# Kernel tuning notes

Hardware: AMD Instinct MI355X
Metric: run time of the kernel (lower is better)

Reference implementation:

```python
import jax, jax.numpy as jnp
import numpy as np
import math

H, D, DEG = 8, 64, 2
GATE_BIAS = 6.906768

def _rope(x, sin, cos):
    # GPT-J style interleaved rotary: even lanes = x1*cos - x2*sin, odd = x2*cos + x1*sin
    x1, x2 = x[..., ::2], x[..., 1::2]
    s = sin[None, :, None, :]
    c = cos[None, :, None, :]
    even = x1 * c - x2 * s
    odd = x2 * c + x1 * s
    return jnp.stack([even, odd], axis=-1).reshape(x.shape)

def _forward(x, w_attn, w_proj):
    B, T, C = x.shape
    h, d, deg = H, D, DEG
    hd = h * d
    scale = 1.0 / math.sqrt(d)
    qkvg = x @ w_attn                                   # (B,T,3hd+h)
    q = qkvg[..., :hd].reshape(B, T, h, d)
    k = qkvg[..., hd:2 * hd].reshape(B, T, h, d)
    v = qkvg[..., 2 * hd:3 * hd].reshape(B, T, h, d)
    log_g = jax.nn.log_sigmoid(GATE_BIAS + qkvg[..., 3 * hd:].astype(jnp.float32))  # (B,T,h)
    # sinusoidal RoPE with frequency 2*pi / T**(2i/d), as in get_sinusoidal_embeddings
    pos = jnp.arange(T, dtype=jnp.float32)
    div = 2.0 * math.pi / (float(T) ** (jnp.arange(0, d, 2, dtype=jnp.float32) / d))
    ang = pos[:, None] * div[None, :]                   # (T, d//2)
    sin, cos = jnp.sin(ang), jnp.cos(ang)
    q = _rope(q, sin, cos)
    k = _rope(k, sin, cos)
    # gated symmetric-power attention: quadratic reference of chunked power_full
    # score_ts = (scale * q_t . k_s)^deg * exp(L_t - L_s), causal, row-normalized
    L = jnp.cumsum(log_g, axis=1).transpose(0, 2, 1)    # (B,h,T) cumulative log-gates
    qk = jnp.einsum('bthd,bshd->bhts', q, k) * scale    # (B,h,T,T)
    log_gate = L[:, :, :, None] - L[:, :, None, :]      # L_t - L_s
    causal = jnp.tril(jnp.ones((T, T), dtype=bool))
    scores = jnp.where(causal, (qk ** deg) * jnp.exp(log_gate), 0.0)
    denom = jnp.maximum(scores.sum(-1, keepdims=True), 1e-6)
    y = jnp.einsum('bhts,bshd->bthd', scores / denom, v)  # (B,T,h,d)
    return y.reshape(B, T, hd) @ w_proj

def setup_inputs() -> dict:
    key = jax.random.key(0)
    k1, k2, k3 = jax.random.split(key, 3)
    B, T, C = 2, 2048, 512
    x = jax.random.normal(k1, (B, T, C), dtype=jnp.float32)
    w_attn = jax.random.normal(k2, (C, 3 * H * D + H), dtype=jnp.float32) * 0.02
    w_proj = jax.random.normal(k3, (H * D, C), dtype=jnp.float32) * 0.02
    return {"x": x, "w_attn": w_attn, "w_proj": w_proj}

def reference(x, w_attn, w_proj):
    return _forward(x, w_attn, w_proj)
```

## Files before the change

kernel.cpp:

```cpp
#include <hip/hip_runtime.h>
#include <math.h>

constexpr int B_ = 2, T_ = 2048, C_ = 512, H_ = 8, D_ = 64;
constexpr int QKVG_ = 3 * H_ * D_ + H_;
constexpr float GATE_BIAS_ = 6.906768f;
constexpr int NPAD1_ = 1664;
constexpr int SC_ = 8;
constexpr int NBLK_ = 1280;
constexpr int MC_ = 4096 * 512;
constexpr int BHT_ = B_ * H_ * T_;

typedef __attribute__((ext_vector_type(8))) short short8;
typedef __attribute__((ext_vector_type(4))) float f32x4;

__device__ __forceinline__ unsigned short f2b(float f) {
    unsigned int u = __float_as_uint(f);
    unsigned int r = (u + 0x7fffu + ((u >> 16) & 1u)) >> 16;
    return (unsigned short)r;
}
__device__ __forceinline__ short8 pack8(float4 a, float4 b) {
    short8 r;
    r[0] = (short)f2b(a.x); r[1] = (short)f2b(a.y);
    r[2] = (short)f2b(a.z); r[3] = (short)f2b(a.w);
    r[4] = (short)f2b(b.x); r[5] = (short)f2b(b.y);
    r[6] = (short)f2b(b.z); r[7] = (short)f2b(b.w);
    return r;
}

__device__ __forceinline__ void gl2lds16(const unsigned short* g, void* lds_base) {
    __builtin_amdgcn_global_load_lds(
        (const __attribute__((address_space(1))) unsigned int*)g,
        (__attribute__((address_space(3))) unsigned int*)lds_base, 16, 0, 0);
}

__device__ __forceinline__ void packT_body(
    const float* __restrict__ W, unsigned short* __restrict__ Bt,
    int K, int N, int nt, int kt, int tid, float (*Ws)[65])
{
    {
        const int r = tid >> 2;
        const int c0 = (tid & 3) * 16;
#pragma unroll
        for (int j = 0; j < 16; ++j) {
            const int n = nt + c0 + j;
            Ws[r][c0 + j] = (n < N) ? W[(size_t)(kt + r) * N + n] : 0.f;
        }
    }
    __syncthreads();
    {
        const int d = tid >> 2;
        const int cc = tid & 3;
        const int kc = cc * 16;
        short8 o0, o1;
#pragma unroll
        for (int j = 0; j < 8; ++j) o0[j] = (short)f2b(Ws[kc + j][d]);
#pragma unroll
        for (int j = 0; j < 8; ++j) o1[j] = (short)f2b(Ws[kc + 8 + j][d]);
        const int row = nt + d;
        unsigned short* op = Bt + (size_t)row * K + kt;
        *(short8*)(op + ((2 * cc) ^ (row & 7)) * 8)     = o0;
        *(short8*)(op + ((2 * cc + 1) ^ (row & 7)) * 8) = o1;
    }
}

__global__ __launch_bounds__(256) void pack_inputs(
    const float* __restrict__ x, const float* __restrict__ w_attn,
    const float* __restrict__ w_proj, unsigned short* __restrict__ xb,
    unsigned short* __restrict__ Bt1, unsigned short* __restrict__ Bt2)
{
    __shared__ float Ws[64][65];
    const int bid = blockIdx.x;
    const int tid = threadIdx.x;
    if (bid < 1024) {
        const int i = bid * 256 + tid;
        float4 f0 = *(const float4*)(x + (size_t)i * 8);
        float4 f1 = *(const float4*)(x + (size_t)i * 8 + 4);
        const int row = i >> 6;
        const int ic = i & 63;
        const int swc = (ic & ~7) | ((ic & 7) ^ (row & 7));
        *(short8*)(xb + (size_t)row * 512 + swc * 8) = pack8(f0, f1);
    } else if (bid < 1232) {
        const int q = bid - 1024;
        packT_body(w_attn, Bt1, C_, QKVG_, (q % 26) * 64, (q / 26) * 64, tid, Ws);
    } else {
        const int q = bid - 1232;
        packT_body(w_proj, Bt2, H_ * D_, C_, (q & 7) * 64, (q >> 3) * 64, tid, Ws);
    }
}

__global__ __launch_bounds__(256) void gemm_bf16(
    const unsigned short* __restrict__ A, const unsigned short* __restrict__ Bt,
    float* __restrict__ C, int M, int N, int K)
{
    __shared__ __align__(16) char AsB[128 * 128];
    __shared__ __align__(16) char BsB[128 * 128];

    const int tid = threadIdx.x;
    const int wave = tid >> 6, lane = tid & 63;
    const int l15 = lane & 15, lhi = lane >> 4;
    const int wr = wave >> 1, wc = wave & 1;
    const int bm = blockIdx.y * 128, bn = blockIdx.x * 128;

    f32x4 acc[4][4];
#pragma unroll
    for (int i = 0; i < 4; ++i)
#pragma unroll
        for (int j = 0; j < 4; ++j) acc[i][j] = (f32x4){0.f, 0.f, 0.f, 0.f};

    const unsigned short* Arow = A + (size_t)bm * K;
    const unsigned short* Brow = Bt + (size_t)bn * K;
    const int sw = (l15 & 7) << 4;

    const int srow = tid >> 3;
    const int schunk = tid & 7;

    for (int k0 = 0; k0 < K; k0 += 64) {
        __syncthreads();
#pragma unroll
        for (int p = 0; p < 4; ++p) {
            const int row = p * 32 + srow;
            const size_t goff = (size_t)row * K + k0 + schunk * 8;
            gl2lds16(Arow + goff, AsB + p * 4096 + wave * 1024);
            gl2lds16(Brow + goff, BsB + p * 4096 + wave * 1024);
        }
        __syncthreads();

        short8 af[4][2];
#pragma unroll
        for (int mi = 0; mi < 4; ++mi) {
            const int row = wr * 64 + mi * 16 + l15;
#pragma unroll
            for (int kk = 0; kk < 2; ++kk)
                af[mi][kk] = *(const short8*)(AsB + row * 128 + ((kk * 64 + lhi * 16) ^ sw));
        }
#pragma unroll
        for (int ni = 0; ni < 4; ++ni) {
            const int row = wc * 64 + ni * 16 + l15;
            short8 bf0 = *(const short8*)(BsB + row * 128 + ((lhi * 16) ^ sw));
            short8 bf1 = *(const short8*)(BsB + row * 128 + ((64 + lhi * 16) ^ sw));
#pragma unroll
            for (int mi = 0; mi < 4; ++mi) {
                acc[mi][ni] = __builtin_amdgcn_mfma_f32_16x16x32_bf16(af[mi][0], bf0, acc[mi][ni], 0, 0, 0);
                acc[mi][ni] = __builtin_amdgcn_mfma_f32_16x16x32_bf16(af[mi][1], bf1, acc[mi][ni], 0, 0, 0);
            }
        }
    }

#pragma unroll
    for (int mi = 0; mi < 4; ++mi) {
        const int gm = bm + wr * 64 + mi * 16 + lhi * 4;
#pragma unroll
        for (int r = 0; r < 4; ++r) {
            float* crow = C + (size_t)(gm + r) * N;
#pragma unroll
            for (int ni = 0; ni < 4; ++ni) {
                const int gn = bn + wc * 64 + ni * 16 + l15;
                if (gn < N) crow[gn] = acc[mi][ni][r];
            }
        }
    }
}

__global__ __launch_bounds__(256) void gate_cumsum(
    const float* __restrict__ qkvg, float* __restrict__ Lg)
{
    __shared__ float wsum[4];
    const int bh = blockIdx.x;
    const int b = bh >> 3, h = bh & 7;
    const int tid = threadIdx.x;
    const int lane = tid & 63, wv = tid >> 6;

    const float* gp = qkvg + (size_t)(b * T_ + tid * 8) * QKVG_ + 1536 + h;
    float v[8];
    float s = 0.f;
#pragma unroll
    for (int j = 0; j < 8; ++j) {
        const float z = gp[(size_t)j * QKVG_] + GATE_BIAS_;
        const float lg = (z > 0.f) ? -log1pf(expf(-z)) : (z - log1pf(expf(z)));
        s += lg;
        v[j] = s;
    }
    float ssum = s;
#pragma unroll
    for (int off = 1; off < 64; off <<= 1) {
        float n = __shfl_up(ssum, off, 64);
        if (lane >= off) ssum += n;
    }
    if (lane == 63) wsum[wv] = ssum;
    __syncthreads();
    float base = ssum - s;
#pragma unroll
    for (int w = 0; w < 3; ++w)
        base += (w < wv) ? wsum[w] : 0.f;

    float* op = Lg + (size_t)bh * T_ + tid * 8;
#pragma unroll
    for (int j = 0; j < 8; ++j) op[j] = v[j] + base;
}

__global__ __launch_bounds__(256) void qkv_pack(
    const float* __restrict__ qkvg, const float* __restrict__ Lg,
    unsigned short* __restrict__ Qsb, unsigned short* __restrict__ Ksb,
    unsigned short* __restrict__ Vtb)
{
    __shared__ float Vs[64][68];
    const int tid = threadIdx.x;
    const int stile = blockIdx.x;
    const int bh = blockIdx.y;
    const int b = bh >> 3, h = bh & 7;
    const int r = tid >> 2, c = tid & 3;
    const int t = stile * 64 + r;

    float sn[8], cs[8];
#pragma unroll
    for (int j = 0; j < 8; ++j) {
        const int i = c * 8 + j;
        const float div = 6.2831853071795864f * exp2f((float)i * (-11.0f / 32.0f));
        const float ang = (float)t * div;
        sn[j] = sinf(ang);
        cs[j] = cosf(ang);
    }

    const float Lt = Lg[(size_t)bh * T_ + t];
    const float eQ = __expf(0.5f * Lt) * 0.125f;
    const float eK = __expf(-0.5f * Lt);
    const float* basep = qkvg + (size_t)(b * T_ + t) * QKVG_ + h * 64 + c * 16;

    {
        float q[16];
        *(float4*)&q[0]  = *(const float4*)(basep + 0);
        *(float4*)&q[4]  = *(const float4*)(basep + 4);
        *(float4*)&q[8]  = *(const float4*)(basep + 8);
        *(float4*)&q[12] = *(const float4*)(basep + 12);
#pragma unroll
        for (int j = 0; j < 8; ++j) {
            const float x1 = q[2 * j], x2 = q[2 * j + 1];
            q[2 * j]     = (x1 * cs[j] - x2 * sn[j]) * eQ;
            q[2 * j + 1] = (x2 * cs[j] + x1 * sn[j]) * eQ;
        }
        unsigned short* op = Qsb + ((size_t)bh * T_ + t) * 64 + c * 16;
        *(short8*)(op + 0) = pack8(*(float4*)&q[0], *(float4*)&q[4]);
        *(short8*)(op + 8) = pack8(*(float4*)&q[8], *(float4*)&q[12]);
    }
    {
        float k[16];
        *(float4*)&k[0]  = *(const float4*)(basep + 512);
        *(float4*)&k[4]  = *(const float4*)(basep + 516);
        *(float4*)&k[8]  = *(const float4*)(basep + 520);
        *(float4*)&k[12] = *(const float4*)(basep + 524);
#pragma unroll
        for (int j = 0; j < 8; ++j) {
            const float x1 = k[2 * j], x2 = k[2 * j + 1];
            k[2 * j]     = (x1 * cs[j] - x2 * sn[j]) * eK;
            k[2 * j + 1] = (x2 * cs[j] + x1 * sn[j]) * eK;
        }
        unsigned short* op = Ksb + ((size_t)bh * T_ + t) * 64;
        *(short8*)(op + ((2 * c) ^ (t & 7)) * 8)     = pack8(*(float4*)&k[0], *(float4*)&k[4]);
        *(short8*)(op + ((2 * c + 1) ^ (t & 7)) * 8) = pack8(*(float4*)&k[8], *(float4*)&k[12]);
    }
    {
        *(float4*)&Vs[r][c * 16 + 0]  = *(const float4*)(basep + 1024);
        *(float4*)&Vs[r][c * 16 + 4]  = *(const float4*)(basep + 1028);
        *(float4*)&Vs[r][c * 16 + 8]  = *(const float4*)(basep + 1032);
        *(float4*)&Vs[r][c * 16 + 12] = *(const float4*)(basep + 1036);
    }
    __syncthreads();
    {
        const int d = tid >> 2, cc = tid & 3;
        short8 o0, o1;
#pragma unroll
        for (int j = 0; j < 8; ++j) o0[j] = (short)f2b(Vs[cc * 16 + j][d]);
#pragma unroll
        for (int j = 0; j < 8; ++j) o1[j] = (short)f2b(Vs[cc * 16 + 8 + j][d]);
        unsigned short* op = Vtb + ((size_t)bh * 64 + d) * T_ + stile * 64;
        *(short8*)(op + ((2 * cc) ^ (d & 7)) * 8)     = o0;
        *(short8*)(op + ((2 * cc + 1) ^ (d & 7)) * 8) = o1;
    }
}

__global__ __launch_bounds__(256) void attn_mfma(
    const unsigned short* __restrict__ Qsb, const unsigned short* __restrict__ Ksb,
    const unsigned short* __restrict__ Vtb,
    float* __restrict__ Y0, float* __restrict__ Yp, float* __restrict__ Dpart)
{
    __shared__ __align__(16) char smem[24576];
    char* KsB = smem;
    char* VtB = smem + 8192;
    char* PsB = smem + 16384;

    const int wg = blockIdx.x;
    const int xcd = wg & 7;
    const int slot = wg >> 3;
    const int bh = (slot < 80) ? xcd : 8 + xcd;
    const int rem = (slot < 80) ? slot : slot - 80;
    const int rr = 79 - rem;
    int bt, sc;
    if (rr < 8)       { bt = rr; sc = 0; }
    else if (rr < 24) { const int q = rr - 8;  bt = 8 + (q >> 1);  sc = q & 1; }
    else if (rr < 48) { const int q = rr - 24; bt = 16 + q / 3;    sc = q % 3; }
    else              { const int q = rr - 48; bt = 24 + (q >> 2); sc = q & 3; }
    const int st0 = sc * SC_;
    const int st1 = min(st0 + SC_ - 1, bt);

    const int tid = threadIdx.x;
    const int wave = tid >> 6;
    const int lane = tid & 63;
    const int l15 = lane & 15;
    const int lhi = lane >> 4;
    const int b = bh >> 3, h = bh & 7;
    const int t0 = bt * 64;

    const int qrow = t0 + wave * 16 + l15;
    const unsigned short* qpp = Qsb + ((size_t)bh * T_ + qrow) * 64 + lhi * 8;
    short8 qf[2];
    qf[0] = *(const short8*)(qpp);
    qf[1] = *(const short8*)(qpp + 32);

    f32x4 accY[4];
#pragma unroll
    for (int n = 0; n < 4; ++n) accY[n] = (f32x4){0.f, 0.f, 0.f, 0.f};
    float den[4] = {0.f, 0.f, 0.f, 0.f};

    const int kchunk = lhi * 16;
    const int rsw = (l15 & 7) << 4;
    const int srow = tid >> 3;
    const int schunk = tid & 7;

    for (int st = st0; st <= st1; ++st) {
        __syncthreads();
#pragma unroll
        for (int p = 0; p < 2; ++p) {
            const int row = p * 32 + srow;
            gl2lds16(Ksb + ((size_t)bh * T_ + st * 64 + row) * 64 + schunk * 8,
                     KsB + p * 4096 + wave * 1024);
            gl2lds16(Vtb + ((size_t)bh * 64 + row) * T_ + st * 64 + schunk * 8,
                     VtB + p * 4096 + wave * 1024);
        }
        __syncthreads();

        f32x4 accS[4];
#pragma unroll
        for (int n = 0; n < 4; ++n) accS[n] = (f32x4){0.f, 0.f, 0.f, 0.f};
#pragma unroll
        for (int n = 0; n < 4; ++n) {
#pragma unroll
            for (int kk = 0; kk < 2; ++kk) {
                short8 bf = *(const short8*)(KsB + (n * 16 + l15) * 128 + ((kk * 64 + kchunk) ^ rsw));
                accS[n] = __builtin_amdgcn_mfma_f32_16x16x32_bf16(qf[kk], bf, accS[n], 0, 0, 0);
            }
        }

        const bool last = (st == bt);
        char* PsW = PsB + wave * 2048;
#pragma unroll
        for (int n = 0; n < 4; ++n) {
#pragma unroll
            for (int r = 0; r < 4; ++r) {
                const float a = accS[n][r];
                float p = a * a;
                if (last)
                    p = ((n * 16 + l15) <= wave * 16 + lhi * 4 + r) ? p : 0.f;
                den[r] += p;
                const int prow = lhi * 4 + r;
                *(unsigned short*)(PsW + prow * 128 + ((2 * (n * 16 + l15)) ^ ((prow & 7) << 4))) = f2b(p);
            }
        }

        short8 pa[2];
#pragma unroll
        for (int kk = 0; kk < 2; ++kk)
            pa[kk] = *(const short8*)(PsW + l15 * 128 + ((kk * 64 + kchunk) ^ rsw));
#pragma unroll
        for (int n = 0; n < 4; ++n) {
#pragma unroll
            for (int kk = 0; kk < 2; ++kk) {
                short8 vb = *(const short8*)(VtB + (n * 16 + l15) * 128 + ((kk * 64 + kchunk) ^ rsw));
                accY[n] = __builtin_amdgcn_mfma_f32_16x16x32_bf16(pa[kk], vb, accY[n], 0, 0, 0);
            }
        }
    }

#pragma unroll
    for (int r = 0; r < 4; ++r) {
        den[r] += __shfl_xor(den[r], 1, 64);
        den[r] += __shfl_xor(den[r], 2, 64);
        den[r] += __shfl_xor(den[r], 4, 64);
        den[r] += __shfl_xor(den[r], 8, 64);
    }

    float* Ybase = (sc == 0) ? Y0 : (Yp + (size_t)(sc - 1) * MC_);
    float* Dbase = Dpart + (size_t)sc * BHT_;
#pragma unroll
    for (int r = 0; r < 4; ++r) {
        const int t = t0 + wave * 16 + lhi * 4 + r;
        if (l15 == 0)
            Dbase[(size_t)bh * T_ + t] = den[r];
        float* yo = Ybase + (size_t)(b * T_ + t) * (H_ * D_) + h * 64 + l15;
#pragma unroll
        for (int n = 0; n < 4; ++n)
            yo[n * 16] = accY[n][r];
    }
}

__global__ __launch_bounds__(256) void normalize_kernel(
    const float* __restrict__ Y0, const float* __restrict__ Yp,
    const float* __restrict__ Dpart, unsigned short* __restrict__ ybb)
{
    const int gid = blockIdx.x * 256 + threadIdx.x;
    const size_t base = (size_t)gid * 8;
    const int row = (int)(base >> 9);
    const int col = (int)(base & 511);
    const int b = row >> 11, t = row & 2047, h = col >> 6;
    const int bh = b * H_ + h;
    const int nsc = ((t >> 6) >> 3) + 1;

    float d = Dpart[(size_t)bh * T_ + t];
    float4 f0 = *(const float4*)(Y0 + base);
    float4 f1 = *(const float4*)(Y0 + base + 4);
    for (int s = 1; s < nsc; ++s) {
        d += Dpart[(size_t)s * BHT_ + (size_t)bh * T_ + t];
        const float* yp = Yp + (size_t)(s - 1) * MC_ + base;
        float4 g0 = *(const float4*)(yp);
        float4 g1 = *(const float4*)(yp + 4);
        f0.x += g0.x; f0.y += g0.y; f0.z += g0.z; f0.w += g0.w;
        f1.x += g1.x; f1.y += g1.y; f1.z += g1.z; f1.w += g1.w;
    }
    const float inv = 1.0f / fmaxf(d, 1e-6f);
    f0.x *= inv; f0.y *= inv; f0.z *= inv; f0.w *= inv;
    f1.x *= inv; f1.y *= inv; f1.z *= inv; f1.w *= inv;

    const int ic = col >> 3;
    const int swc = (ic & ~7) | ((ic & 7) ^ (row & 7));
    *(short8*)(ybb + (size_t)row * 512 + swc * 8) = pack8(f0, f1);
}

extern "C" void kernel_launch(void* const* d_in, const int* in_sizes, int n_in,
                              void* d_out, int out_size, void* d_ws, size_t ws_size,
                              hipStream_t stream)
{
    const float* x      = (const float*)d_in[0];
    const float* w_attn = (const float*)d_in[1];
    const float* w_proj = (const float*)d_in[2];
    float* out = (float*)d_out;

    float* qkvg = (float*)d_ws;
    float* Lg    = qkvg + (size_t)B_ * T_ * QKVG_;
    float* Dpart = Lg + BHT_;
    unsigned short* Vtb = (unsigned short*)(Dpart + 4 * BHT_);
    unsigned short* Bt1 = Vtb + (size_t)B_ * H_ * D_ * T_;
    unsigned short* Bt2 = Bt1 + (size_t)NPAD1_ * C_;
    unsigned short* xb  = Bt2 + (size_t)C_ * C_;
    unsigned short* Ksb = xb;
    unsigned short* ybb = xb;
    float* Yp = (float*)(xb + (size_t)MC_);
    unsigned short* Qsb = (unsigned short*)(Yp + 3 * (size_t)MC_);

    const int M = B_ * T_;

    pack_inputs<<<1296, 256, 0, stream>>>(x, w_attn, w_proj, xb, Bt1, Bt2);

    gemm_bf16<<<dim3(NPAD1_ / 128, M / 128), 256, 0, stream>>>(
        xb, Bt1, qkvg, M, QKVG_, C_);

    gate_cumsum<<<B_ * H_, 256, 0, stream>>>(qkvg, Lg);

    qkv_pack<<<dim3(T_ / 64, B_ * H_), 256, 0, stream>>>(qkvg, Lg, Qsb, Ksb, Vtb);

    attn_mfma<<<NBLK_, 256, 0, stream>>>(Qsb, Ksb, Vtb, out, Yp, Dpart);

    normalize_kernel<<<(MC_ / 8) / 256, 256, 0, stream>>>(out, Yp, Dpart, ybb);

    gemm_bf16<<<dim3(C_ / 128, M / 128), 256, 0, stream>>>(
        ybb, Bt2, out, M, C_, H_ * D_);
}
```

Before: 89.60 us.

## Fuse RoPE, gate scaling and QKV packing into the QKV GEMM epilogue

The gate projection is computed separately in fp32 inside the pack kernel, and a sin/cos table is precomputed there. The gate cumsum now runs before the QKV GEMM, which applies RoPE, the exp(±L/2) scaling and the bf16 packing of Q/K/V directly in its epilogue. This drops the fp32 qkvg intermediate and the separate qkv_pack launch, and the N padding shrinks from 1664 to 1536. In exchange the GEMM epilogue gets heavier, with two LDS staging rounds, and the gate GEMV re-reads x in fp32.

Result: faster. 84.24 us (-6.0%).

```diff
diff --git a/kernel.cpp b/kernel.cpp
--- a/kernel.cpp
+++ b/kernel.cpp
@@ -4,7 +4,7 @@
 constexpr int B_ = 2, T_ = 2048, C_ = 512, H_ = 8, D_ = 64;
 constexpr int QKVG_ = 3 * H_ * D_ + H_;
 constexpr float GATE_BIAS_ = 6.906768f;
-constexpr int NPAD1_ = 1664;
+constexpr int N1_ = 1536;
 constexpr int SC_ = 8;
 constexpr int NBLK_ = 1280;
 constexpr int MC_ = 4096 * 512;
@@ -35,7 +35,7 @@
 
 __device__ __forceinline__ void packT_body(
     const float* __restrict__ W, unsigned short* __restrict__ Bt,
-    int K, int N, int nt, int kt, int tid, float (*Ws)[65])
+    int K, int N, int ldW, int nt, int kt, int tid, float (*Ws)[65])
 {
     {
         const int r = tid >> 2;
@@ -43,7 +43,7 @@
 #pragma unroll
         for (int j = 0; j < 16; ++j) {
             const int n = nt + c0 + j;
-            Ws[r][c0 + j] = (n < N) ? W[(size_t)(kt + r) * N + n] : 0.f;
+            Ws[r][c0 + j] = (n < N) ? W[(size_t)(kt + r) * ldW + n] : 0.f;
         }
     }
     __syncthreads();
@@ -66,9 +66,11 @@
 __global__ __launch_bounds__(256) void pack_inputs(
     const float* __restrict__ x, const float* __restrict__ w_attn,
     const float* __restrict__ w_proj, unsigned short* __restrict__ xb,
-    unsigned short* __restrict__ Bt1, unsigned short* __restrict__ Bt2)
-{
-    __shared__ float Ws[64][65];
+    unsigned short* __restrict__ Bt1, unsigned short* __restrict__ Bt2,
+    float2* __restrict__ sincos, float* __restrict__ g)
+{
+    __shared__ float SM[64 * 65];
+    float (*Ws)[65] = (float(*)[65])SM;
     const int bid = blockIdx.x;
     const int tid = threadIdx.x;
     if (bid < 1024) {
@@ -79,21 +81,98 @@
         const int ic = i & 63;
         const int swc = (ic & ~7) | ((ic & 7) ^ (row & 7));
         *(short8*)(xb + (size_t)row * 512 + swc * 8) = pack8(f0, f1);
-    } else if (bid < 1232) {
+    } else if (bid < 1216) {
         const int q = bid - 1024;
-        packT_body(w_attn, Bt1, C_, QKVG_, (q % 26) * 64, (q / 26) * 64, tid, Ws);
+        packT_body(w_attn, Bt1, C_, N1_, QKVG_, (q % 24) * 64, (q / 24) * 64, tid, Ws);
+    } else if (bid < 1280) {
+        const int q = bid - 1216;
+        packT_body(w_proj, Bt2, H_ * D_, C_, C_, (q & 7) * 64, (q >> 3) * 64, tid, Ws);
+    } else if (bid < 1288) {
+        const int t = (bid - 1280) * 256 + tid;
+        float2* op = sincos + (size_t)t * 32;
+#pragma unroll
+        for (int i = 0; i < 32; ++i) {
+            const float div = 6.2831853071795864f * exp2f((float)i * (-11.0f / 32.0f));
+            const float ang = (float)t * div;
+            op[i] = make_float2(cosf(ang), sinf(ang));
+        }
     } else {
-        const int q = bid - 1232;
-        packT_body(w_proj, Bt2, H_ * D_, C_, (q & 7) * 64, (q >> 3) * 64, tid, Ws);
-    }
-}
-
-__global__ __launch_bounds__(256) void gemm_bf16(
+        const int q = bid - 1288;
+        float* LDSw = SM;
+        {
+            const int k = tid * 2;
+#pragma unroll
+            for (int kk = 0; kk < 2; ++kk) {
+                const float* wp = w_attn + (size_t)(k + kk) * QKVG_ + 1536;
+                float4 wa = *(const float4*)wp;
+                float4 wb = *(const float4*)(wp + 4);
+                float* dst = LDSw + (k + kk) * 8;
+                *(float4*)dst = wa;
+                *(float4*)(dst + 4) = wb;
+            }
+        }
+        __syncthreads();
+        const int m = q * 32 + (tid >> 3);
+        const int h = tid & 7;
+        const float* xrow = x + (size_t)m * C_;
+        float s = 0.f;
+#pragma unroll 4
+        for (int k0 = 0; k0 < 512; k0 += 4) {
+            float4 xv = *(const float4*)(xrow + k0);
+            s += xv.x * LDSw[(k0 + 0) * 8 + h] + xv.y * LDSw[(k0 + 1) * 8 + h]
+               + xv.z * LDSw[(k0 + 2) * 8 + h] + xv.w * LDSw[(k0 + 3) * 8 + h];
+        }
+        const int b = m >> 11, t = m & 2047;
+        g[(size_t)(b * 8 + h) * T_ + t] = s;
+    }
+}
+
+__global__ __launch_bounds__(256) void gate_cumsum(
+    const float* __restrict__ g, float* __restrict__ Lg)
+{
+    __shared__ float wsum[4];
+    const int bh = blockIdx.x;
+    const int tid = threadIdx.x;
+    const int lane = tid & 63, wv = tid >> 6;
+
+    const float* gp = g + (size_t)bh * T_ + tid * 8;
+    float v[8];
+    float s = 0.f;
+#pragma unroll
+    for (int j = 0; j < 8; ++j) {
+        const float z = gp[j] + GATE_BIAS_;
+        const float lg = (z > 0.f) ? -log1pf(expf(-z)) : (z - log1pf(expf(z)));
+        s += lg;
+        v[j] = s;
+    }
+    float ssum = s;
+#pragma unroll
+    for (int off = 1; off < 64; off <<= 1) {
+        float n = __shfl_up(ssum, off, 64);
+        if (lane >= off) ssum += n;
+    }
+    if (lane == 63) wsum[wv] = ssum;
+    __syncthreads();
+    float base = ssum - s;
+#pragma unroll
+    for (int w = 0; w < 3; ++w)
+        base += (w < wv) ? wsum[w] : 0.f;
+
+    float* op = Lg + (size_t)bh * T_ + tid * 8;
+#pragma unroll
+    for (int j = 0; j < 8; ++j) op[j] = v[j] + base;
+}
+
+__global__ __launch_bounds__(256) void gemm_fused(
     const unsigned short* __restrict__ A, const unsigned short* __restrict__ Bt,
-    float* __restrict__ C, int M, int N, int K)
-{
-    __shared__ __align__(16) char AsB[128 * 128];
-    __shared__ __align__(16) char BsB[128 * 128];
+    const float* __restrict__ Lg, const float2* __restrict__ sincos,
+    unsigned short* __restrict__ Qsb, unsigned short* __restrict__ Ksb,
+    unsigned short* __restrict__ Vtb)
+{
+    __shared__ __align__(16) char smem[33280];
+    char* AsB = smem;
+    char* BsB = smem + 16384;
+    float (*epi)[65] = (float(*)[65])smem;
 
     const int tid = threadIdx.x;
     const int wave = tid >> 6, lane = tid & 63;
@@ -107,10 +186,130 @@
 #pragma unroll
         for (int j = 0; j < 4; ++j) acc[i][j] = (f32x4){0.f, 0.f, 0.f, 0.f};
 
+    const unsigned short* Arow = A + (size_t)bm * C_;
+    const unsigned short* Brow = Bt + (size_t)bn * C_;
+    const int sw = (l15 & 7) << 4;
+    const int srow = tid >> 3;
+    const int schunk = tid & 7;
+
+    for (int k0 = 0; k0 < C_; k0 += 64) {
+        __syncthreads();
+#pragma unroll
+        for (int p = 0; p < 4; ++p) {
+            const int row = p * 32 + srow;
+            const size_t goff = (size_t)row * C_ + k0 + schunk * 8;
+            gl2lds16(Arow + goff, AsB + p * 4096 + wave * 1024);
+            gl2lds16(Brow + goff, BsB + p * 4096 + wave * 1024);
+        }
+        __syncthreads();
+
+        short8 af[4][2];
+#pragma unroll
+        for (int mi = 0; mi < 4; ++mi) {
+            const int row = wr * 64 + mi * 16 + l15;
+#pragma unroll
+            for (int kk = 0; kk < 2; ++kk)
+                af[mi][kk] = *(const short8*)(AsB + row * 128 + ((kk * 64 + lhi * 16) ^ sw));
+        }
+#pragma unroll
+        for (int ni = 0; ni < 4; ++ni) {
+            const int row = wc * 64 + ni * 16 + l15;
+            short8 bf0 = *(const short8*)(BsB + row * 128 + ((lhi * 16) ^ sw));
+            short8 bf1 = *(const short8*)(BsB + row * 128 + ((64 + lhi * 16) ^ sw));
+#pragma unroll
+            for (int mi = 0; mi < 4; ++mi) {
+                acc[mi][ni] = __builtin_amdgcn_mfma_f32_16x16x32_bf16(af[mi][0], bf0, acc[mi][ni], 0, 0, 0);
+                acc[mi][ni] = __builtin_amdgcn_mfma_f32_16x16x32_bf16(af[mi][1], bf1, acc[mi][ni], 0, 0, 0);
+            }
+        }
+    }
+
+    const int rid = bn >> 9;
+    const int b = bm >> 11;
+    const int tloc0 = bm & 2047;
+
+#pragma unroll
+    for (int hc = 0; hc < 2; ++hc) {
+        __syncthreads();
+        if (wc == hc) {
+#pragma unroll
+            for (int mi = 0; mi < 4; ++mi)
+#pragma unroll
+                for (int ni = 0; ni < 4; ++ni)
+#pragma unroll
+                    for (int r = 0; r < 4; ++r)
+                        epi[wr * 64 + mi * 16 + lhi * 4 + r][ni * 16 + l15] = acc[mi][ni][r];
+        }
+        __syncthreads();
+        const int h = ((bn & 511) >> 6) + hc;
+        const int bh = b * 8 + h;
+        if (rid < 2) {
+            const int row = tid >> 1;
+            const int c0 = (tid & 1) * 32;
+            const int t = tloc0 + row;
+            const float Lt = Lg[(size_t)bh * T_ + t];
+            const float scl = (rid == 0) ? (__expf(0.5f * Lt) * 0.125f)
+                                         : __expf(-0.5f * Lt);
+            float vb[32];
+#pragma unroll
+            for (int j = 0; j < 32; ++j) vb[j] = epi[row][c0 + j];
+            const float2* sct = sincos + (size_t)t * 32 + (c0 >> 1);
+#pragma unroll
+            for (int p = 0; p < 16; ++p) {
+                const float2 cssn = sct[p];
+                const float x1 = vb[2 * p], x2 = vb[2 * p + 1];
+                vb[2 * p]     = (x1 * cssn.x - x2 * cssn.y) * scl;
+                vb[2 * p + 1] = (x2 * cssn.x + x1 * cssn.y) * scl;
+            }
+            unsigned short* op = ((rid == 0) ? Qsb : Ksb) + ((size_t)bh * T_ + t) * 64;
+#pragma unroll
+            for (int j = 0; j < 4; ++j) {
+                short8 o = pack8(*(float4*)&vb[j * 8], *(float4*)&vb[j * 8 + 4]);
+                const int chunk = (c0 >> 3) + j;
+                const int pos = (rid == 0) ? chunk : (chunk ^ (t & 7));
+                *(short8*)(op + pos * 8) = o;
+            }
+        } else {
+            const int d = tid >> 2;
+            const int tq = tid & 3;
+            unsigned short* op = Vtb + ((size_t)(bh * 64 + d)) * T_;
+#pragma unroll
+            for (int j = 0; j < 4; ++j) {
+                const int tl = tq * 32 + j * 8;
+                short8 o;
+#pragma unroll
+                for (int e = 0; e < 8; ++e)
+                    o[e] = (short)f2b(epi[tl + e][d]);
+                const int chunkidx = (tloc0 + tl) >> 3;
+                const int pos = (chunkidx & ~7) | ((chunkidx & 7) ^ (d & 7));
+                *(short8*)(op + pos * 8) = o;
+            }
+        }
+    }
+}
+
+__global__ __launch_bounds__(256) void gemm_bf16(
+    const unsigned short* __restrict__ A, const unsigned short* __restrict__ Bt,
+    float* __restrict__ C, int M, int N, int K)
+{
+    __shared__ __align__(16) char AsB[128 * 128];
+    __shared__ __align__(16) char BsB[128 * 128];
+
+    const int tid = threadIdx.x;
+    const int wave = tid >> 6, lane = tid & 63;
+    const int l15 = lane & 15, lhi = lane >> 4;
+    const int wr = wave >> 1, wc = wave & 1;
+    const int bm = blockIdx.y * 128, bn = blockIdx.x * 128;
+
+    f32x4 acc[4][4];
+#pragma unroll
+    for (int i = 0; i < 4; ++i)
+#pragma unroll
+        for (int j = 0; j < 4; ++j) acc[i][j] = (f32x4){0.f, 0.f, 0.f, 0.f};
+
     const unsigned short* Arow = A + (size_t)bm * K;
     const unsigned short* Brow = Bt + (size_t)bn * K;
     const int sw = (l15 & 7) << 4;
-
     const int srow = tid >> 3;
     const int schunk = tid & 7;
 
@@ -158,123 +357,6 @@
                 if (gn < N) crow[gn] = acc[mi][ni][r];
             }
         }
-    }
-}
-
-__global__ __launch_bounds__(256) void gate_cumsum(
-    const float* __restrict__ qkvg, float* __restrict__ Lg)
-{
-    __shared__ float wsum[4];
-    const int bh = blockIdx.x;
-    const int b = bh >> 3, h = bh & 7;
-    const int tid = threadIdx.x;
-    const int lane = tid & 63, wv = tid >> 6;
-
-    const float* gp = qkvg + (size_t)(b * T_ + tid * 8) * QKVG_ + 1536 + h;
-    float v[8];
-    float s = 0.f;
-#pragma unroll
-    for (int j = 0; j < 8; ++j) {
-        const float z = gp[(size_t)j * QKVG_] + GATE_BIAS_;
-        const float lg = (z > 0.f) ? -log1pf(expf(-z)) : (z - log1pf(expf(z)));
-        s += lg;
-        v[j] = s;
-    }
-    float ssum = s;
-#pragma unroll
-    for (int off = 1; off < 64; off <<= 1) {
-        float n = __shfl_up(ssum, off, 64);
-        if (lane >= off) ssum += n;
-    }
-    if (lane == 63) wsum[wv] = ssum;
-    __syncthreads();
-    float base = ssum - s;
-#pragma unroll
-    for (int w = 0; w < 3; ++w)
-        base += (w < wv) ? wsum[w] : 0.f;
-
-    float* op = Lg + (size_t)bh * T_ + tid * 8;
-#pragma unroll
-    for (int j = 0; j < 8; ++j) op[j] = v[j] + base;
-}
-
-__global__ __launch_bounds__(256) void qkv_pack(
-    const float* __restrict__ qkvg, const float* __restrict__ Lg,
-    unsigned short* __restrict__ Qsb, unsigned short* __restrict__ Ksb,
-    unsigned short* __restrict__ Vtb)
-{
-    __shared__ float Vs[64][68];
-    const int tid = threadIdx.x;
-    const int stile = blockIdx.x;
-    const int bh = blockIdx.y;
-    const int b = bh >> 3, h = bh & 7;
-    const int r = tid >> 2, c = tid & 3;
-    const int t = stile * 64 + r;
-
-    float sn[8], cs[8];
-#pragma unroll
-    for (int j = 0; j < 8; ++j) {
-        const int i = c * 8 + j;
-        const float div = 6.2831853071795864f * exp2f((float)i * (-11.0f / 32.0f));
-        const float ang = (float)t * div;
-        sn[j] = sinf(ang);
-        cs[j] = cosf(ang);
-    }
-
-    const float Lt = Lg[(size_t)bh * T_ + t];
-    const float eQ = __expf(0.5f * Lt) * 0.125f;
-    const float eK = __expf(-0.5f * Lt);
-    const float* basep = qkvg + (size_t)(b * T_ + t) * QKVG_ + h * 64 + c * 16;
-
-    {
-        float q[16];
-        *(float4*)&q[0]  = *(const float4*)(basep + 0);
-        *(float4*)&q[4]  = *(const float4*)(basep + 4);
-        *(float4*)&q[8]  = *(const float4*)(basep + 8);
-        *(float4*)&q[12] = *(const float4*)(basep + 12);
-#pragma unroll
-        for (int j = 0; j < 8; ++j) {
-            const float x1 = q[2 * j], x2 = q[2 * j + 1];
-            q[2 * j]     = (x1 * cs[j] - x2 * sn[j]) * eQ;
-            q[2 * j + 1] = (x2 * cs[j] + x1 * sn[j]) * eQ;
-        }
-        unsigned short* op = Qsb + ((size_t)bh * T_ + t) * 64 + c * 16;
-        *(short8*)(op + 0) = pack8(*(float4*)&q[0], *(float4*)&q[4]);
-        *(short8*)(op + 8) = pack8(*(float4*)&q[8], *(float4*)&q[12]);
-    }
-    {
-        float k[16];
-        *(float4*)&k[0]  = *(const float4*)(basep + 512);
-        *(float4*)&k[4]  = *(const float4*)(basep + 516);
-        *(float4*)&k[8]  = *(const float4*)(basep + 520);
-        *(float4*)&k[12] = *(const float4*)(basep + 524);
-#pragma unroll
-        for (int j = 0; j < 8; ++j) {
-            const float x1 = k[2 * j], x2 = k[2 * j + 1];
-            k[2 * j]     = (x1 * cs[j] - x2 * sn[j]) * eK;
-            k[2 * j + 1] = (x2 * cs[j] + x1 * sn[j]) * eK;
-        }
-        unsigned short* op = Ksb + ((size_t)bh * T_ + t) * 64;
-        *(short8*)(op + ((2 * c) ^ (t & 7)) * 8)     = pack8(*(float4*)&k[0], *(float4*)&k[4]);
-        *(short8*)(op + ((2 * c + 1) ^ (t & 7)) * 8) = pack8(*(float4*)&k[8], *(float4*)&k[12]);
-    }
-    {
-        *(float4*)&Vs[r][c * 16 + 0]  = *(const float4*)(basep + 1024);
-        *(float4*)&Vs[r][c * 16 + 4]  = *(const float4*)(basep + 1028);
-        *(float4*)&Vs[r][c * 16 + 8]  = *(const float4*)(basep + 1032);
-        *(float4*)&Vs[r][c * 16 + 12] = *(const float4*)(basep + 1036);
-    }
-    __syncthreads();
-    {
-        const int d = tid >> 2, cc = tid & 3;
-        short8 o0, o1;
-#pragma unroll
-        for (int j = 0; j < 8; ++j) o0[j] = (short)f2b(Vs[cc * 16 + j][d]);
-#pragma unroll
-        for (int j = 0; j < 8; ++j) o1[j] = (short)f2b(Vs[cc * 16 + 8 + j][d]);
-        unsigned short* op = Vtb + ((size_t)bh * 64 + d) * T_ + stile * 64;
-        *(short8*)(op + ((2 * cc) ^ (d & 7)) * 8)     = o0;
-        *(short8*)(op + ((2 * cc + 1) ^ (d & 7)) * 8) = o1;
     }
 }
 
@@ -443,28 +525,28 @@
     const float* w_proj = (const float*)d_in[2];
     float* out = (float*)d_out;
 
-    float* qkvg = (float*)d_ws;
-    float* Lg    = qkvg + (size_t)B_ * T_ * QKVG_;
-    float* Dpart = Lg + BHT_;
-    unsigned short* Vtb = (unsigned short*)(Dpart + 4 * BHT_);
-    unsigned short* Bt1 = Vtb + (size_t)B_ * H_ * D_ * T_;
-    unsigned short* Bt2 = Bt1 + (size_t)NPAD1_ * C_;
-    unsigned short* xb  = Bt2 + (size_t)C_ * C_;
-    unsigned short* Ksb = xb;
-    unsigned short* ybb = xb;
-    float* Yp = (float*)(xb + (size_t)MC_);
-    unsigned short* Qsb = (unsigned short*)(Yp + 3 * (size_t)MC_);
+    char* p = (char*)d_ws;
+    float2* sincos = (float2*)p;               p += (size_t)T_ * 32 * 8;
+    float* g       = (float*)p;                p += (size_t)BHT_ * 4;
+    float* Lg      = (float*)p;                p += (size_t)BHT_ * 4;
+    float* Dpart   = (float*)p;                p += (size_t)4 * BHT_ * 4;
+    unsigned short* xb  = (unsigned short*)p;  p += (size_t)MC_ * 2;
+    unsigned short* Bt1 = (unsigned short*)p;  p += (size_t)N1_ * C_ * 2;
+    unsigned short* Bt2 = (unsigned short*)p;  p += (size_t)C_ * C_ * 2;
+    unsigned short* Qsb = (unsigned short*)p;  p += (size_t)BHT_ * 64 * 2;
+    unsigned short* Ksb = (unsigned short*)p;  p += (size_t)BHT_ * 64 * 2;
+    unsigned short* Vtb = (unsigned short*)p;  p += (size_t)BHT_ * 64 * 2;
+    float* Yp      = (float*)p;                p += (size_t)3 * MC_ * 4;
+    unsigned short* ybb = (unsigned short*)p;
 
     const int M = B_ * T_;
 
-    pack_inputs<<<1296, 256, 0, stream>>>(x, w_attn, w_proj, xb, Bt1, Bt2);
-
-    gemm_bf16<<<dim3(NPAD1_ / 128, M / 128), 256, 0, stream>>>(
-        xb, Bt1, qkvg, M, QKVG_, C_);
-
-    gate_cumsum<<<B_ * H_, 256, 0, stream>>>(qkvg, Lg);
-
-    qkv_pack<<<dim3(T_ / 64, B_ * H_), 256, 0, stream>>>(qkvg, Lg, Qsb, Ksb, Vtb);
+    pack_inputs<<<1416, 256, 0, stream>>>(x, w_attn, w_proj, xb, Bt1, Bt2, sincos, g);
+
+    gate_cumsum<<<B_ * H_, 256, 0, stream>>>(g, Lg);
+
+    gemm_fused<<<dim3(N1_ / 128, M / 128), 256, 0, stream>>>(
+        xb, Bt1, Lg, sincos, Qsb, Ksb, Vtb);
 
     attn_mfma<<<NBLK_, 256, 0, stream>>>(Qsb, Ksb, Vtb, out, Yp, Dpart);
 
```
